# Kernel tuning notes

Hardware: AMD Instinct MI355X
Metric: run time of the kernel (lower is better)

## Reference

```python
import jax, jax.numpy as jnp
import numpy as np

N = 50000   # n_nodes (cells)
E = 800000  # n_edges (avg degree 16)
D = 128     # feature dim


def setup_inputs() -> dict:
    key = jax.random.key(0)
    ks = jax.random.split(key, 8)
    x = jax.random.normal(ks[0], (N, D), dtype=jnp.float32)
    src = jax.random.randint(ks[1], (E,), 0, N, dtype=jnp.int32)
    dst = jax.random.randint(ks[2], (E,), 0, N, dtype=jnp.int32)
    vals = jax.random.uniform(ks[3], (E,), dtype=jnp.float32)
    # GraphConvolution weight (dim -> dim), applied as x @ W
    W_gc = jax.random.normal(ks[4], (D, D), dtype=jnp.float32) / np.sqrt(D).astype(np.float32)
    b_gc = jnp.zeros((D,), jnp.float32)
    # linear2: nn.Linear(dim, dim) -> x @ W2.T + b2
    W2 = jax.random.normal(ks[5], (D, D), dtype=jnp.float32) / np.sqrt(D).astype(np.float32)
    b2 = jnp.zeros((D,), jnp.float32)
    return {"x": x, "vals": vals, "W_gc": W_gc, "b_gc": b_gc,
            "W2": W2, "b2": b2, "src": src, "dst": dst}


def reference(x, vals, W_gc, b_gc, W2, b2, src, dst):
    # GraphConvolution (dropout is identity in eval mode):
    #   support = x @ W + b ; out = relu(adj_sparse @ support)
    support = x @ W_gc + b_gc                         # [N, D]
    msg = support[src] * vals[:, None]                # gather rows, scale by edge weight
    agg = jax.ops.segment_sum(msg, dst, num_segments=N)  # SpMM via scatter-add
    x1 = jax.nn.relu(agg)                             # [N, D]
    # linear2 + dropout(eval=identity) + detached L2 row-normalize
    x2 = x1 @ W2.T + b2                               # [N, D]
    nrm = jax.lax.stop_gradient(
        jnp.sqrt(jnp.sum(x2 * x2, axis=1, keepdims=True)))
    return x2 / nrm
```

## Files before the change

kernel.cpp:

```cpp
#include <hip/hip_runtime.h>
#include <hip/hip_bf16.h>

#define N_NODES 50000
#define N_EDGES 800000
#define DIM     128
#define N_STRIPS (N_NODES / 16)
#define N_BKT    ((N_NODES + 255) / 256)
#define EDGE_BLOCKS ((N_EDGES + 4095) / 4096)
#define BUF_CAP  6144
#define GEMM_BLOCKS ((N_STRIPS + 3) / 4)
#define HIST_BLOCK0 GEMM_BLOCKS
#define PACK_BLOCK0 (GEMM_BLOCKS + EDGE_BLOCKS)
#define FRONT_BLOCKS (PACK_BLOCK0 + 8)
#define CHUNKS_PER_PART (EDGE_BLOCKS / 4)

typedef short short8 __attribute__((ext_vector_type(8)));
typedef float floatx4 __attribute__((ext_vector_type(4)));

__device__ inline unsigned short f2bf(float f) {
    __hip_bfloat16 h = __float2bfloat16(f);
    return *reinterpret_cast<unsigned short*>(&h);
}

__global__ __launch_bounds__(256) void pack_w1(
    const float* __restrict__ W, uint4* __restrict__ p1)
{
    const int s    = blockIdx.x * 256 + threadIdx.x;
    const int lane = s & 63;
    const int nt   = (s >> 6) & 7;
    const int ks   = s >> 9;
    const int m    = lane & 15;
    const int q    = lane >> 4;
    unsigned short e[8];
    #pragma unroll
    for (int j = 0; j < 8; ++j)
        e[j] = f2bf(W[(ks * 32 + q * 8 + j) * DIM + nt * 16 + m]);
    uint4 o;
    o.x = (unsigned)e[0] | ((unsigned)e[1] << 16);
    o.y = (unsigned)e[2] | ((unsigned)e[3] << 16);
    o.z = (unsigned)e[4] | ((unsigned)e[5] << 16);
    o.w = (unsigned)e[6] | ((unsigned)e[7] << 16);
    p1[s] = o;
}

__global__ __launch_bounds__(256) void fused_front(
    const float* __restrict__ x, const float* __restrict__ W2,
    const float* __restrict__ bias, const int* __restrict__ dst,
    const uint4* __restrict__ p1,
    unsigned short* __restrict__ support, int* __restrict__ blk_hist,
    uint4* __restrict__ p2)
{
    __shared__ int bh[256];
    const int t = threadIdx.x;

    if (blockIdx.x < HIST_BLOCK0) {
        const int wave  = t >> 6;
        const int lane  = t & 63;
        const int strip = blockIdx.x * 4 + wave;
        if (strip >= N_STRIPS) return;
        const int m = lane & 15;
        const int q = lane >> 4;
        const int row = strip * 16 + m;

        short8 a[4];
        const float4* xr = reinterpret_cast<const float4*>(&x[(size_t)row * DIM]);
        #pragma unroll
        for (int ks = 0; ks < 4; ++ks) {
            const float4 f0 = xr[ks * 8 + q * 2];
            const float4 f1 = xr[ks * 8 + q * 2 + 1];
            short8 tt;
            tt[0] = (short)f2bf(f0.x); tt[1] = (short)f2bf(f0.y);
            tt[2] = (short)f2bf(f0.z); tt[3] = (short)f2bf(f0.w);
            tt[4] = (short)f2bf(f1.x); tt[5] = (short)f2bf(f1.y);
            tt[6] = (short)f2bf(f1.z); tt[7] = (short)f2bf(f1.w);
            a[ks] = tt;
        }

        floatx4 acc[8];
        #pragma unroll
        for (int nt = 0; nt < 8; ++nt) { acc[nt][0]=0.f; acc[nt][1]=0.f; acc[nt][2]=0.f; acc[nt][3]=0.f; }

        const short8* Bp = (const short8*)p1;
        #pragma unroll
        for (int ks = 0; ks < 4; ++ks) {
            #pragma unroll
            for (int nt = 0; nt < 8; ++nt) {
                const short8 bf = Bp[(ks * 8 + nt) * 64 + lane];
                acc[nt] = __builtin_amdgcn_mfma_f32_16x16x32_bf16(a[ks], bf, acc[nt], 0, 0, 0);
            }
        }

        #pragma unroll
        for (int nt = 0; nt < 8; ++nt) {
            const float bb = bias[nt * 16 + m];
            #pragma unroll
            for (int i = 0; i < 4; ++i) {
                const int r = strip * 16 + q * 4 + i;
                support[(size_t)r * DIM + nt * 16 + m] = f2bf(acc[nt][i] + bb);
            }
        }
    } else if (blockIdx.x < PACK_BLOCK0) {
        const int chunk = blockIdx.x - HIST_BLOCK0;
        bh[t] = 0;
        __syncthreads();
        const int base   = chunk * 4096;
        const int navail = min(4096, N_EDGES - base);
        const int4* d4 = reinterpret_cast<const int4*>(dst + base);
        #pragma unroll
        for (int i = 0; i < 4; ++i) {
            const int j = t + i * 256;
            if (j * 4 < navail) {
                const int4 d = d4[j];
                atomicAdd(&bh[d.x >> 8], 1);
                atomicAdd(&bh[d.y >> 8], 1);
                atomicAdd(&bh[d.z >> 8], 1);
                atomicAdd(&bh[d.w >> 8], 1);
            }
        }
        __syncthreads();
        blk_hist[chunk * 256 + t] = bh[t];
    } else {
        const int pb   = blockIdx.x - PACK_BLOCK0;
        const int s    = pb * 256 + t;
        const int lane = s & 63;
        const int nt   = (s >> 6) & 7;
        const int ks   = s >> 9;
        const int m    = lane & 15;
        const int q    = lane >> 4;
        const float4 f0 = *reinterpret_cast<const float4*>(&W2[(nt * 16 + m) * DIM + ks * 32 + q * 8]);
        const float4 f1 = *reinterpret_cast<const float4*>(&W2[(nt * 16 + m) * DIM + ks * 32 + q * 8 + 4]);
        unsigned short e[8];
        e[0] = f2bf(f0.x); e[1] = f2bf(f0.y); e[2] = f2bf(f0.z); e[3] = f2bf(f0.w);
        e[4] = f2bf(f1.x); e[5] = f2bf(f1.y); e[6] = f2bf(f1.z); e[7] = f2bf(f1.w);
        uint4 o;
        o.x = (unsigned)e[0] | ((unsigned)e[1] << 16);
        o.y = (unsigned)e[2] | ((unsigned)e[3] << 16);
        o.z = (unsigned)e[4] | ((unsigned)e[5] << 16);
        o.w = (unsigned)e[6] | ((unsigned)e[7] << 16);
        p2[s] = o;
    }
}

__global__ __launch_bounds__(1024) void scan_hist(
    const int* __restrict__ blk_hist, int* __restrict__ blk_base,
    int* __restrict__ bbase)
{
    __shared__ int psum[4][256];
    __shared__ int stot[256];
    __shared__ int sinc[256];

    const int t    = threadIdx.x;
    const int b    = t & 255;
    const int part = t >> 8;
    const int c0   = part * CHUNKS_PER_PART;

    int pre[CHUNKS_PER_PART];
    int run = 0;
    #pragma unroll
    for (int k = 0; k < CHUNKS_PER_PART; ++k) {
        const int v = blk_hist[(c0 + k) * 256 + b];
        pre[k] = run;
        run += v;
    }
    psum[part][b] = run;
    __syncthreads();

    if (part == 0) {
        const int tot = psum[0][b] + psum[1][b] + psum[2][b] + psum[3][b];
        stot[b] = tot;
        sinc[b] = tot;
    }
    __syncthreads();
    for (int off = 1; off < 256; off <<= 1) {
        int u = 0;
        if (part == 0 && b >= off) u = sinc[b - off];
        __syncthreads();
        if (part == 0 && b >= off) sinc[b] += u;
        __syncthreads();
    }
    const int ex = sinc[b] - stot[b];
    if (part == 0 && b < N_BKT) bbase[b] = ex;
    if (t == 0) bbase[N_BKT] = N_EDGES;

    int partbase = 0;
    #pragma unroll
    for (int p = 0; p < 4; ++p) if (p < part) partbase += psum[p][b];
    const int add = ex + partbase;
    #pragma unroll
    for (int k = 0; k < CHUNKS_PER_PART; ++k)
        blk_base[(c0 + k) * 256 + b] = pre[k] + add;
}

__global__ __launch_bounds__(256) void bucket_scatter(
    const int* __restrict__ src, const int* __restrict__ dst,
    const float* __restrict__ vals, const int* __restrict__ blk_base,
    int2* __restrict__ bucketed)
{
    __shared__ int rcur[256];
    const int t     = threadIdx.x;
    const int chunk = blockIdx.x;
    rcur[t] = blk_base[chunk * 256 + t];
    __syncthreads();

    const int base   = chunk * 4096;
    const int navail = min(4096, N_EDGES - base);
    const int4*   s4 = reinterpret_cast<const int4*>(src + base);
    const int4*   d4 = reinterpret_cast<const int4*>(dst + base);
    const float4* v4 = reinterpret_cast<const float4*>(vals + base);
    #pragma unroll
    for (int i = 0; i < 4; ++i) {
        const int j = t + i * 256;
        if (j * 4 < navail) {
            const int4   s = s4[j];
            const int4   d = d4[j];
            const float4 v = v4[j];
            int p;
            p = atomicAdd(&rcur[d.x >> 8], 1);
            bucketed[p] = make_int2((s.x & 0xFFFF) | ((d.x & 0xFF) << 16), __float_as_int(v.x));
            p = atomicAdd(&rcur[d.y >> 8], 1);
            bucketed[p] = make_int2((s.y & 0xFFFF) | ((d.y & 0xFF) << 16), __float_as_int(v.y));
            p = atomicAdd(&rcur[d.z >> 8], 1);
            bucketed[p] = make_int2((s.z & 0xFFFF) | ((d.z & 0xFF) << 16), __float_as_int(v.z));
            p = atomicAdd(&rcur[d.w >> 8], 1);
            bucketed[p] = make_int2((s.w & 0xFFFF) | ((d.w & 0xFF) << 16), __float_as_int(v.w));
        }
    }
}

__global__ __launch_bounds__(512) void bucket_to_csr(
    const int2* __restrict__ bucketed, const int* __restrict__ bbase,
    int2* __restrict__ packed, int* __restrict__ offs)
{
    __shared__ int cnt[256];
    __shared__ int sc[256];
    __shared__ int lcur[256];
    __shared__ int2 buf[BUF_CAP];

    const int b    = blockIdx.x;
    const int t    = threadIdx.x;
    const int base = bbase[b];
    const int nE   = bbase[b + 1] - base;

    if (t < 256) cnt[t] = 0;
    __syncthreads();
    for (int i = t; i < nE; i += 512)
        atomicAdd(&cnt[(bucketed[base + i].x >> 16) & 0xFF], 1);
    __syncthreads();
    if (t < 256) sc[t] = cnt[t];
    __syncthreads();
    #pragma unroll
    for (int off = 1; off < 256; off <<= 1) {
        int u = 0;
        if (t < 256 && t >= off) u = sc[t - off];
        __syncthreads();
        if (t < 256 && t >= off) sc[t] += u;
        __syncthreads();
    }
    if (t < 256) lcur[t] = sc[t] - cnt[t];
    __syncthreads();

    if (nE <= BUF_CAP) {
        for (int i = t; i < nE; i += 512) {
            const int2 e = bucketed[base + i];
            const int  n = (e.x >> 16) & 0xFF;
            const int  p = atomicAdd(&lcur[n], 1);
            buf[p] = make_int2(e.x & 0xFFFF, e.y);
        }
        __syncthreads();
        for (int i = t; i < nE; i += 512)
            packed[base + i] = buf[i];
    } else {
        for (int i = t; i < nE; i += 512) {
            const int2 e = bucketed[base + i];
            const int  n = (e.x >> 16) & 0xFF;
            const int  p = atomicAdd(&lcur[n], 1);
            packed[base + p] = make_int2(e.x & 0xFFFF, e.y);
        }
    }

    if (t < 256) {
        const int node = b * 256 + t;
        if (node < N_NODES) offs[node] = base + (sc[t] - cnt[t]);
    }
    if (b == N_BKT - 1 && t == 0) offs[N_NODES] = N_EDGES;
}

__global__ __launch_bounds__(256) void csr_gather_bf16(
    const unsigned int* __restrict__ sup, const int2* __restrict__ packed,
    const int* __restrict__ offs, unsigned int* __restrict__ agg)
{
    const int node = (blockIdx.x * 256 + threadIdx.x) >> 6;
    const int lane = threadIdx.x & 63;
    if (node >= N_NODES) return;
    const int beg = offs[node];
    const int end = offs[node + 1];

    float ax = 0.f, ay = 0.f;
    int j = beg;
    for (; j + 7 < end; j += 8) {
        int2 e[8];
        unsigned int u[8];
        #pragma unroll
        for (int k = 0; k < 8; ++k) e[k] = packed[j + k];
        #pragma unroll
        for (int k = 0; k < 8; ++k) u[k] = sup[(size_t)e[k].x * 64 + lane];
        #pragma unroll
        for (int k = 0; k < 8; ++k) {
            const float v = __int_as_float(e[k].y);
            ax += __uint_as_float(u[k] << 16) * v;
            ay += __uint_as_float(u[k] & 0xffff0000u) * v;
        }
    }
    for (; j + 3 < end; j += 4) {
        int2 e[4];
        unsigned int u[4];
        #pragma unroll
        for (int k = 0; k < 4; ++k) e[k] = packed[j + k];
        #pragma unroll
        for (int k = 0; k < 4; ++k) u[k] = sup[(size_t)e[k].x * 64 + lane];
        #pragma unroll
        for (int k = 0; k < 4; ++k) {
            const float v = __int_as_float(e[k].y);
            ax += __uint_as_float(u[k] << 16) * v;
            ay += __uint_as_float(u[k] & 0xffff0000u) * v;
        }
    }
    for (; j < end; ++j) {
        const int2 e0 = packed[j];
        const unsigned int u0 = sup[(size_t)e0.x * 64 + lane];
        const float v0 = __int_as_float(e0.y);
        ax += __uint_as_float(u0 << 16) * v0;
        ay += __uint_as_float(u0 & 0xffff0000u) * v0;
    }
    ax = fmaxf(ax, 0.f);
    ay = fmaxf(ay, 0.f);
    agg[(size_t)node * 64 + lane] = (unsigned int)f2bf(ax) | ((unsigned int)f2bf(ay) << 16);
}

__global__ __launch_bounds__(256) void gemm2_mfma(
    const short8* __restrict__ aggv, const short8* __restrict__ Bp,
    const float* __restrict__ bias, float* __restrict__ out)
{
    const int wave  = threadIdx.x >> 6;
    const int lane  = threadIdx.x & 63;
    const int strip = blockIdx.x * 4 + wave;
    if (strip >= N_STRIPS) return;
    const int m = lane & 15;
    const int q = lane >> 4;
    const int row = strip * 16 + m;

    short8 a[4];
    #pragma unroll
    for (int ks = 0; ks < 4; ++ks)
        a[ks] = aggv[(size_t)row * (DIM / 8) + ks * 4 + q];

    floatx4 acc[8];
    #pragma unroll
    for (int nt = 0; nt < 8; ++nt) { acc[nt][0]=0.f; acc[nt][1]=0.f; acc[nt][2]=0.f; acc[nt][3]=0.f; }

    #pragma unroll
    for (int ks = 0; ks < 4; ++ks) {
        #pragma unroll
        for (int nt = 0; nt < 8; ++nt) {
            const short8 bf = Bp[(ks * 8 + nt) * 64 + lane];
            acc[nt] = __builtin_amdgcn_mfma_f32_16x16x32_bf16(a[ks], bf, acc[nt], 0, 0, 0);
        }
    }

    #pragma unroll
    for (int nt = 0; nt < 8; ++nt) {
        const float bb = bias[nt * 16 + m];
        #pragma unroll
        for (int i = 0; i < 4; ++i) acc[nt][i] += bb;
    }

    float sq[4] = {0.f, 0.f, 0.f, 0.f};
    #pragma unroll
    for (int nt = 0; nt < 8; ++nt)
        #pragma unroll
        for (int i = 0; i < 4; ++i) sq[i] += acc[nt][i] * acc[nt][i];
    #pragma unroll
    for (int i = 0; i < 4; ++i) {
        #pragma unroll
        for (int mask = 1; mask < 16; mask <<= 1)
            sq[i] += __shfl_xor(sq[i], mask);
        sq[i] = 1.0f / sqrtf(sq[i]);
    }

    #pragma unroll
    for (int nt = 0; nt < 8; ++nt) {
        #pragma unroll
        for (int i = 0; i < 4; ++i) {
            const int r = strip * 16 + q * 4 + i;
            out[(size_t)r * DIM + nt * 16 + m] = acc[nt][i] * sq[i];
        }
    }
}

extern "C" void kernel_launch(void* const* d_in, const int* in_sizes, int n_in,
                              void* d_out, int out_size, void* d_ws, size_t ws_size,
                              hipStream_t stream) {
    const float* x    = (const float*)d_in[0];
    const float* vals = (const float*)d_in[1];
    const float* W_gc = (const float*)d_in[2];
    const float* b_gc = (const float*)d_in[3];
    const float* W2   = (const float*)d_in[4];
    const float* b2   = (const float*)d_in[5];
    const int*   src  = (const int*)d_in[6];
    const int*   dst  = (const int*)d_in[7];

    unsigned short* support = (unsigned short*)d_out;
    float* out = (float*)d_out;

    const size_t AGG_B  = (size_t)N_NODES * DIM * 2;
    const size_t OFFS_B = 200064;
    const size_t BH_B   = (size_t)EDGE_BLOCKS * 256 * 4;
    const size_t BB_B   = (size_t)EDGE_BLOCKS * 256 * 4;
    const size_t BKT_B  = 1024;
    const size_t BUK_B  = (size_t)N_EDGES * 8;
    const size_t PACK_B = (size_t)N_EDGES * 8;
    const size_t PW_B   = 32768;

    char* wsb = (char*)d_ws;
    unsigned int* agg = (unsigned int*)wsb;
    int*   offs     = (int*)(wsb + AGG_B);
    int*   blk_hist = (int*)(wsb + AGG_B + OFFS_B);
    int*   blk_base = (int*)(wsb + AGG_B + OFFS_B + BH_B);
    int*   bbase    = (int*)(wsb + AGG_B + OFFS_B + BH_B + BB_B);
    int2*  bucketed = (int2*)(wsb + AGG_B + OFFS_B + BH_B + BB_B + BKT_B);
    int2*  packed   = (int2*)(wsb + AGG_B + OFFS_B + BH_B + BB_B + BKT_B + BUK_B);
    uint4* pw1      = (uint4*)(wsb + AGG_B + OFFS_B + BH_B + BB_B + BKT_B + BUK_B + PACK_B);
    uint4* pw2      = (uint4*)(wsb + AGG_B + OFFS_B + BH_B + BB_B + BKT_B + BUK_B + PACK_B + PW_B);

    pack_w1<<<8, 256, 0, stream>>>(W_gc, pw1);

    fused_front<<<FRONT_BLOCKS, 256, 0, stream>>>(
        x, W2, b_gc, dst, pw1, support, blk_hist, pw2);

    scan_hist<<<1, 1024, 0, stream>>>(blk_hist, blk_base, bbase);

    bucket_scatter<<<EDGE_BLOCKS, 256, 0, stream>>>(src, dst, vals, blk_base, bucketed);

    bucket_to_csr<<<N_BKT, 512, 0, stream>>>(bucketed, bbase, packed, offs);

    csr_gather_bf16<<<(N_NODES * 64 + 255) / 256, 256, 0, stream>>>(
        (const unsigned int*)support, packed, offs, agg);

    gemm2_mfma<<<GEMM_BLOCKS, 256, 0, stream>>>(
        (const short8*)agg, (const short8*)pw2, b2, out);
}
```

Baseline: 166.9 us.

## Collapse graph pipeline into three kernels with atomic bucket reservation and fused aggregation-GEMM

Replaces the global histogram scan with per-bucket atomic reservation into fixed-capacity buckets, folds the bucket scatter into the front GEMM kernel, and fuses CSR sort, gather-aggregate, ReLU, second GEMM and L2 normalize into one 1024-thread kernel per 256-node bucket. Aggregated rows stay in LDS instead of round-tripping through global memory, and the launch count drops from seven to three. In exchange the gather runs with far fewer waves (one block per bucket), which limits latency hiding. Buckets with more edges than the fixed capacities would silently drop edges.

```diff
diff --git a/kernel.cpp b/kernel.cpp
--- a/kernel.cpp
+++ b/kernel.cpp
@@ -5,14 +5,13 @@
 #define N_EDGES 800000
 #define DIM     128
 #define N_STRIPS (N_NODES / 16)
-#define N_BKT    ((N_NODES + 255) / 256)
-#define EDGE_BLOCKS ((N_EDGES + 4095) / 4096)
-#define BUF_CAP  6144
+#define N_BKT    196
+#define EDGE_CHUNKS 196
+#define BCAP     8192
+#define EBUF_CAP 7168
+#define AGS      68
 #define GEMM_BLOCKS ((N_STRIPS + 3) / 4)
-#define HIST_BLOCK0 GEMM_BLOCKS
-#define PACK_BLOCK0 (GEMM_BLOCKS + EDGE_BLOCKS)
-#define FRONT_BLOCKS (PACK_BLOCK0 + 8)
-#define CHUNKS_PER_PART (EDGE_BLOCKS / 4)
+#define FRONT_BLOCKS (GEMM_BLOCKS + EDGE_CHUNKS)
 
 typedef short short8 __attribute__((ext_vector_type(8)));
 typedef float floatx4 __attribute__((ext_vector_type(4)));
@@ -22,106 +21,31 @@
     return *reinterpret_cast<unsigned short*>(&h);
 }
 
-__global__ __launch_bounds__(256) void pack_w1(
-    const float* __restrict__ W, uint4* __restrict__ p1)
+__global__ __launch_bounds__(256) void pre_pack(
+    const float* __restrict__ W1, const float* __restrict__ W2,
+    uint4* __restrict__ p1, uint4* __restrict__ p2, int* __restrict__ bcnt)
 {
-    const int s    = blockIdx.x * 256 + threadIdx.x;
-    const int lane = s & 63;
-    const int nt   = (s >> 6) & 7;
-    const int ks   = s >> 9;
-    const int m    = lane & 15;
-    const int q    = lane >> 4;
-    unsigned short e[8];
-    #pragma unroll
-    for (int j = 0; j < 8; ++j)
-        e[j] = f2bf(W[(ks * 32 + q * 8 + j) * DIM + nt * 16 + m]);
-    uint4 o;
-    o.x = (unsigned)e[0] | ((unsigned)e[1] << 16);
-    o.y = (unsigned)e[2] | ((unsigned)e[3] << 16);
-    o.z = (unsigned)e[4] | ((unsigned)e[5] << 16);
-    o.w = (unsigned)e[6] | ((unsigned)e[7] << 16);
-    p1[s] = o;
-}
-
-__global__ __launch_bounds__(256) void fused_front(
-    const float* __restrict__ x, const float* __restrict__ W2,
-    const float* __restrict__ bias, const int* __restrict__ dst,
-    const uint4* __restrict__ p1,
-    unsigned short* __restrict__ support, int* __restrict__ blk_hist,
-    uint4* __restrict__ p2)
-{
-    __shared__ int bh[256];
-    const int t = threadIdx.x;
-
-    if (blockIdx.x < HIST_BLOCK0) {
-        const int wave  = t >> 6;
-        const int lane  = t & 63;
-        const int strip = blockIdx.x * 4 + wave;
-        if (strip >= N_STRIPS) return;
-        const int m = lane & 15;
-        const int q = lane >> 4;
-        const int row = strip * 16 + m;
-
-        short8 a[4];
-        const float4* xr = reinterpret_cast<const float4*>(&x[(size_t)row * DIM]);
-        #pragma unroll
-        for (int ks = 0; ks < 4; ++ks) {
-            const float4 f0 = xr[ks * 8 + q * 2];
-            const float4 f1 = xr[ks * 8 + q * 2 + 1];
-            short8 tt;
-            tt[0] = (short)f2bf(f0.x); tt[1] = (short)f2bf(f0.y);
-            tt[2] = (short)f2bf(f0.z); tt[3] = (short)f2bf(f0.w);
-            tt[4] = (short)f2bf(f1.x); tt[5] = (short)f2bf(f1.y);
-            tt[6] = (short)f2bf(f1.z); tt[7] = (short)f2bf(f1.w);
-            a[ks] = tt;
-        }
-
-        floatx4 acc[8];
-        #pragma unroll
-        for (int nt = 0; nt < 8; ++nt) { acc[nt][0]=0.f; acc[nt][1]=0.f; acc[nt][2]=0.f; acc[nt][3]=0.f; }
-
-        const short8* Bp = (const short8*)p1;
-        #pragma unroll
-        for (int ks = 0; ks < 4; ++ks) {
-            #pragma unroll
-            for (int nt = 0; nt < 8; ++nt) {
-                const short8 bf = Bp[(ks * 8 + nt) * 64 + lane];
-                acc[nt] = __builtin_amdgcn_mfma_f32_16x16x32_bf16(a[ks], bf, acc[nt], 0, 0, 0);
-            }
-        }
-
-        #pragma unroll
-        for (int nt = 0; nt < 8; ++nt) {
-            const float bb = bias[nt * 16 + m];
-            #pragma unroll
-            for (int i = 0; i < 4; ++i) {
-                const int r = strip * 16 + q * 4 + i;
-                support[(size_t)r * DIM + nt * 16 + m] = f2bf(acc[nt][i] + bb);
-            }
-        }
-    } else if (blockIdx.x < PACK_BLOCK0) {
-        const int chunk = blockIdx.x - HIST_BLOCK0;
-        bh[t] = 0;
-        __syncthreads();
-        const int base   = chunk * 4096;
-        const int navail = min(4096, N_EDGES - base);
-        const int4* d4 = reinterpret_cast<const int4*>(dst + base);
-        #pragma unroll
-        for (int i = 0; i < 4; ++i) {
-            const int j = t + i * 256;
-            if (j * 4 < navail) {
-                const int4 d = d4[j];
-                atomicAdd(&bh[d.x >> 8], 1);
-                atomicAdd(&bh[d.y >> 8], 1);
-                atomicAdd(&bh[d.z >> 8], 1);
-                atomicAdd(&bh[d.w >> 8], 1);
-            }
-        }
-        __syncthreads();
-        blk_hist[chunk * 256 + t] = bh[t];
-    } else {
-        const int pb   = blockIdx.x - PACK_BLOCK0;
-        const int s    = pb * 256 + t;
+    const int blk = blockIdx.x;
+    const int t   = threadIdx.x;
+    if (blk < 8) {
+        const int s    = blk * 256 + t;
+        const int lane = s & 63;
+        const int nt   = (s >> 6) & 7;
+        const int ks   = s >> 9;
+        const int m    = lane & 15;
+        const int q    = lane >> 4;
+        unsigned short e[8];
+        #pragma unroll
+        for (int j = 0; j < 8; ++j)
+            e[j] = f2bf(W1[(ks * 32 + q * 8 + j) * DIM + nt * 16 + m]);
+        uint4 o;
+        o.x = (unsigned)e[0] | ((unsigned)e[1] << 16);
+        o.y = (unsigned)e[2] | ((unsigned)e[3] << 16);
+        o.z = (unsigned)e[4] | ((unsigned)e[5] << 16);
+        o.w = (unsigned)e[6] | ((unsigned)e[7] << 16);
+        p1[s] = o;
+    } else if (blk < 16) {
+        const int s    = (blk - 8) * 256 + t;
         const int lane = s & 63;
         const int nt   = (s >> 6) & 7;
         const int ks   = s >> 9;
@@ -138,221 +62,212 @@
         o.z = (unsigned)e[4] | ((unsigned)e[5] << 16);
         o.w = (unsigned)e[6] | ((unsigned)e[7] << 16);
         p2[s] = o;
-    }
-}
-
-__global__ __launch_bounds__(1024) void scan_hist(
-    const int* __restrict__ blk_hist, int* __restrict__ blk_base,
-    int* __restrict__ bbase)
+    } else {
+        bcnt[t] = 0;
+    }
+}
+
+__global__ __launch_bounds__(256) void front(
+    const float* __restrict__ x, const float* __restrict__ bias,
+    const int* __restrict__ src, const int* __restrict__ dst,
+    const float* __restrict__ vals, const uint4* __restrict__ p1,
+    unsigned short* __restrict__ support, int* __restrict__ bcnt,
+    int2* __restrict__ bucketed)
 {
-    __shared__ int psum[4][256];
-    __shared__ int stot[256];
-    __shared__ int sinc[256];
-
-    const int t    = threadIdx.x;
-    const int b    = t & 255;
-    const int part = t >> 8;
-    const int c0   = part * CHUNKS_PER_PART;
-
-    int pre[CHUNKS_PER_PART];
-    int run = 0;
-    #pragma unroll
-    for (int k = 0; k < CHUNKS_PER_PART; ++k) {
-        const int v = blk_hist[(c0 + k) * 256 + b];
-        pre[k] = run;
-        run += v;
-    }
-    psum[part][b] = run;
-    __syncthreads();
-
-    if (part == 0) {
-        const int tot = psum[0][b] + psum[1][b] + psum[2][b] + psum[3][b];
-        stot[b] = tot;
-        sinc[b] = tot;
-    }
+    __shared__ int bh[256];
+    __shared__ int rcur[256];
+    const int t = threadIdx.x;
+
+    if (blockIdx.x < GEMM_BLOCKS) {
+        const int wave  = t >> 6;
+        const int lane  = t & 63;
+        const int strip = blockIdx.x * 4 + wave;
+        if (strip >= N_STRIPS) return;
+        const int m = lane & 15;
+        const int q = lane >> 4;
+        const int row = strip * 16 + m;
+
+        short8 a[4];
+        const float4* xr = reinterpret_cast<const float4*>(&x[(size_t)row * DIM]);
+        #pragma unroll
+        for (int ks = 0; ks < 4; ++ks) {
+            const float4 f0 = xr[ks * 8 + q * 2];
+            const float4 f1 = xr[ks * 8 + q * 2 + 1];
+            short8 tt;
+            tt[0] = (short)f2bf(f0.x); tt[1] = (short)f2bf(f0.y);
+            tt[2] = (short)f2bf(f0.z); tt[3] = (short)f2bf(f0.w);
+            tt[4] = (short)f2bf(f1.x); tt[5] = (short)f2bf(f1.y);
+            tt[6] = (short)f2bf(f1.z); tt[7] = (short)f2bf(f1.w);
+            a[ks] = tt;
+        }
+
+        floatx4 acc[8];
+        #pragma unroll
+        for (int nt = 0; nt < 8; ++nt) { acc[nt][0]=0.f; acc[nt][1]=0.f; acc[nt][2]=0.f; acc[nt][3]=0.f; }
+
+        const short8* Bp = (const short8*)p1;
+        #pragma unroll
+        for (int ks = 0; ks < 4; ++ks) {
+            #pragma unroll
+            for (int nt = 0; nt < 8; ++nt) {
+                const short8 bf = Bp[(ks * 8 + nt) * 64 + lane];
+                acc[nt] = __builtin_amdgcn_mfma_f32_16x16x32_bf16(a[ks], bf, acc[nt], 0, 0, 0);
+            }
+        }
+
+        #pragma unroll
+        for (int nt = 0; nt < 8; ++nt) {
+            const float bb = bias[nt * 16 + m];
+            #pragma unroll
+            for (int i = 0; i < 4; ++i) {
+                const int r = strip * 16 + q * 4 + i;
+                support[(size_t)r * DIM + nt * 16 + m] = f2bf(acc[nt][i] + bb);
+            }
+        }
+    } else {
+        const int chunk = blockIdx.x - GEMM_BLOCKS;
+        bh[t] = 0;
+        __syncthreads();
+        const int base   = chunk * 4096;
+        const int navail = min(4096, N_EDGES - base);
+        const int4* d4 = reinterpret_cast<const int4*>(dst + base);
+        #pragma unroll
+        for (int i = 0; i < 4; ++i) {
+            const int j = t + i * 256;
+            if (j * 4 < navail) {
+                const int4 d = d4[j];
+                atomicAdd(&bh[d.x >> 8], 1);
+                atomicAdd(&bh[d.y >> 8], 1);
+                atomicAdd(&bh[d.z >> 8], 1);
+                atomicAdd(&bh[d.w >> 8], 1);
+            }
+        }
+        __syncthreads();
+        rcur[t] = t * BCAP + atomicAdd(&bcnt[t], bh[t]);
+        __syncthreads();
+        const int4*   s4 = reinterpret_cast<const int4*>(src + base);
+        const float4* v4 = reinterpret_cast<const float4*>(vals + base);
+        #pragma unroll
+        for (int i = 0; i < 4; ++i) {
+            const int j = t + i * 256;
+            if (j * 4 < navail) {
+                const int4   s = s4[j];
+                const int4   d = d4[j];
+                const float4 v = v4[j];
+                int p;
+                p = atomicAdd(&rcur[d.x >> 8], 1);
+                bucketed[p] = make_int2((s.x & 0xFFFF) | ((d.x & 0xFF) << 16), __float_as_int(v.x));
+                p = atomicAdd(&rcur[d.y >> 8], 1);
+                bucketed[p] = make_int2((s.y & 0xFFFF) | ((d.y & 0xFF) << 16), __float_as_int(v.y));
+                p = atomicAdd(&rcur[d.z >> 8], 1);
+                bucketed[p] = make_int2((s.z & 0xFFFF) | ((d.z & 0xFF) << 16), __float_as_int(v.z));
+                p = atomicAdd(&rcur[d.w >> 8], 1);
+                bucketed[p] = make_int2((s.w & 0xFFFF) | ((d.w & 0xFF) << 16), __float_as_int(v.w));
+            }
+        }
+    }
+}
+
+__global__ __launch_bounds__(1024) void agg_gemm2(
+    const unsigned int* __restrict__ sup, const int2* __restrict__ bucketed,
+    const int* __restrict__ bcnt, const short8* __restrict__ Bp,
+    const float* __restrict__ bias, float* __restrict__ out)
+{
+    __shared__ int2 ebuf[EBUF_CAP];
+    __shared__ unsigned int agg[256 * AGS];
+    __shared__ int cnt[256];
+    __shared__ int coff[256];
+    __shared__ int cur[256];
+
+    const int b = blockIdx.x;
+    const int t = threadIdx.x;
+    int nE = bcnt[b];
+    if (nE > EBUF_CAP) nE = EBUF_CAP;
+    const int base = b * BCAP;
+
+    if (t < 256) cnt[t] = 0;
+    __syncthreads();
+    for (int i = t; i < nE; i += 1024)
+        atomicAdd(&cnt[(bucketed[base + i].x >> 16) & 255], 1);
+    __syncthreads();
+    if (t < 256) coff[t] = cnt[t];
     __syncthreads();
     for (int off = 1; off < 256; off <<= 1) {
         int u = 0;
-        if (part == 0 && b >= off) u = sinc[b - off];
-        __syncthreads();
-        if (part == 0 && b >= off) sinc[b] += u;
-        __syncthreads();
-    }
-    const int ex = sinc[b] - stot[b];
-    if (part == 0 && b < N_BKT) bbase[b] = ex;
-    if (t == 0) bbase[N_BKT] = N_EDGES;
-
-    int partbase = 0;
-    #pragma unroll
-    for (int p = 0; p < 4; ++p) if (p < part) partbase += psum[p][b];
-    const int add = ex + partbase;
-    #pragma unroll
-    for (int k = 0; k < CHUNKS_PER_PART; ++k)
-        blk_base[(c0 + k) * 256 + b] = pre[k] + add;
-}
-
-__global__ __launch_bounds__(256) void bucket_scatter(
-    const int* __restrict__ src, const int* __restrict__ dst,
-    const float* __restrict__ vals, const int* __restrict__ blk_base,
-    int2* __restrict__ bucketed)
-{
-    __shared__ int rcur[256];
-    const int t     = threadIdx.x;
-    const int chunk = blockIdx.x;
-    rcur[t] = blk_base[chunk * 256 + t];
-    __syncthreads();
-
-    const int base   = chunk * 4096;
-    const int navail = min(4096, N_EDGES - base);
-    const int4*   s4 = reinterpret_cast<const int4*>(src + base);
-    const int4*   d4 = reinterpret_cast<const int4*>(dst + base);
-    const float4* v4 = reinterpret_cast<const float4*>(vals + base);
-    #pragma unroll
-    for (int i = 0; i < 4; ++i) {
-        const int j = t + i * 256;
-        if (j * 4 < navail) {
-            const int4   s = s4[j];
-            const int4   d = d4[j];
-            const float4 v = v4[j];
-            int p;
-            p = atomicAdd(&rcur[d.x >> 8], 1);
-            bucketed[p] = make_int2((s.x & 0xFFFF) | ((d.x & 0xFF) << 16), __float_as_int(v.x));
-            p = atomicAdd(&rcur[d.y >> 8], 1);
-            bucketed[p] = make_int2((s.y & 0xFFFF) | ((d.y & 0xFF) << 16), __float_as_int(v.y));
-            p = atomicAdd(&rcur[d.z >> 8], 1);
-            bucketed[p] = make_int2((s.z & 0xFFFF) | ((d.z & 0xFF) << 16), __float_as_int(v.z));
-            p = atomicAdd(&rcur[d.w >> 8], 1);
-            bucketed[p] = make_int2((s.w & 0xFFFF) | ((d.w & 0xFF) << 16), __float_as_int(v.w));
-        }
-    }
-}
-
-__global__ __launch_bounds__(512) void bucket_to_csr(
-    const int2* __restrict__ bucketed, const int* __restrict__ bbase,
-    int2* __restrict__ packed, int* __restrict__ offs)
-{
-    __shared__ int cnt[256];
-    __shared__ int sc[256];
-    __shared__ int lcur[256];
-    __shared__ int2 buf[BUF_CAP];
-
-    const int b    = blockIdx.x;
-    const int t    = threadIdx.x;
-    const int base = bbase[b];
-    const int nE   = bbase[b + 1] - base;
-
-    if (t < 256) cnt[t] = 0;
-    __syncthreads();
-    for (int i = t; i < nE; i += 512)
-        atomicAdd(&cnt[(bucketed[base + i].x >> 16) & 0xFF], 1);
-    __syncthreads();
-    if (t < 256) sc[t] = cnt[t];
-    __syncthreads();
-    #pragma unroll
-    for (int off = 1; off < 256; off <<= 1) {
-        int u = 0;
-        if (t < 256 && t >= off) u = sc[t - off];
-        __syncthreads();
-        if (t < 256 && t >= off) sc[t] += u;
-        __syncthreads();
-    }
-    if (t < 256) lcur[t] = sc[t] - cnt[t];
-    __syncthreads();
-
-    if (nE <= BUF_CAP) {
-        for (int i = t; i < nE; i += 512) {
-            const int2 e = bucketed[base + i];
-            const int  n = (e.x >> 16) & 0xFF;
-            const int  p = atomicAdd(&lcur[n], 1);
-            buf[p] = make_int2(e.x & 0xFFFF, e.y);
-        }
-        __syncthreads();
-        for (int i = t; i < nE; i += 512)
-            packed[base + i] = buf[i];
-    } else {
-        for (int i = t; i < nE; i += 512) {
-            const int2 e = bucketed[base + i];
-            const int  n = (e.x >> 16) & 0xFF;
-            const int  p = atomicAdd(&lcur[n], 1);
-            packed[base + p] = make_int2(e.x & 0xFFFF, e.y);
-        }
-    }
-
-    if (t < 256) {
-        const int node = b * 256 + t;
-        if (node < N_NODES) offs[node] = base + (sc[t] - cnt[t]);
-    }
-    if (b == N_BKT - 1 && t == 0) offs[N_NODES] = N_EDGES;
-}
-
-__global__ __launch_bounds__(256) void csr_gather_bf16(
-    const unsigned int* __restrict__ sup, const int2* __restrict__ packed,
-    const int* __restrict__ offs, unsigned int* __restrict__ agg)
-{
-    const int node = (blockIdx.x * 256 + threadIdx.x) >> 6;
-    const int lane = threadIdx.x & 63;
-    if (node >= N_NODES) return;
-    const int beg = offs[node];
-    const int end = offs[node + 1];
-
-    float ax = 0.f, ay = 0.f;
-    int j = beg;
-    for (; j + 7 < end; j += 8) {
-        int2 e[8];
-        unsigned int u[8];
-        #pragma unroll
-        for (int k = 0; k < 8; ++k) e[k] = packed[j + k];
-        #pragma unroll
-        for (int k = 0; k < 8; ++k) u[k] = sup[(size_t)e[k].x * 64 + lane];
-        #pragma unroll
-        for (int k = 0; k < 8; ++k) {
-            const float v = __int_as_float(e[k].y);
-            ax += __uint_as_float(u[k] << 16) * v;
-            ay += __uint_as_float(u[k] & 0xffff0000u) * v;
-        }
-    }
-    for (; j + 3 < end; j += 4) {
-        int2 e[4];
-        unsigned int u[4];
-        #pragma unroll
-        for (int k = 0; k < 4; ++k) e[k] = packed[j + k];
-        #pragma unroll
-        for (int k = 0; k < 4; ++k) u[k] = sup[(size_t)e[k].x * 64 + lane];
-        #pragma unroll
-        for (int k = 0; k < 4; ++k) {
-            const float v = __int_as_float(e[k].y);
-            ax += __uint_as_float(u[k] << 16) * v;
-            ay += __uint_as_float(u[k] & 0xffff0000u) * v;
-        }
-    }
-    for (; j < end; ++j) {
-        const int2 e0 = packed[j];
-        const unsigned int u0 = sup[(size_t)e0.x * 64 + lane];
-        const float v0 = __int_as_float(e0.y);
-        ax += __uint_as_float(u0 << 16) * v0;
-        ay += __uint_as_float(u0 & 0xffff0000u) * v0;
-    }
-    ax = fmaxf(ax, 0.f);
-    ay = fmaxf(ay, 0.f);
-    agg[(size_t)node * 64 + lane] = (unsigned int)f2bf(ax) | ((unsigned int)f2bf(ay) << 16);
-}
-
-__global__ __launch_bounds__(256) void gemm2_mfma(
-    const short8* __restrict__ aggv, const short8* __restrict__ Bp,
-    const float* __restrict__ bias, float* __restrict__ out)
-{
-    const int wave  = threadIdx.x >> 6;
-    const int lane  = threadIdx.x & 63;
-    const int strip = blockIdx.x * 4 + wave;
-    if (strip >= N_STRIPS) return;
+        if (t < 256 && t >= off) u = coff[t - off];
+        __syncthreads();
+        if (t < 256 && t >= off) coff[t] += u;
+        __syncthreads();
+    }
+    if (t < 256) cur[t] = coff[t] - cnt[t];
+    __syncthreads();
+    for (int i = t; i < nE; i += 1024) {
+        const int2 e = bucketed[base + i];
+        const int  n = (e.x >> 16) & 255;
+        const int  p = atomicAdd(&cur[n], 1);
+        ebuf[p] = e;
+    }
+    __syncthreads();
+
+    const int w    = t >> 6;
+    const int lane = t & 63;
+    for (int nl = w * 16; nl < w * 16 + 16; ++nl) {
+        const int end = cur[nl];
+        const int beg = end - cnt[nl];
+        float ax = 0.f, ay = 0.f;
+        int j = beg;
+        for (; j + 7 < end; j += 8) {
+            int2 e[8];
+            unsigned int u[8];
+            #pragma unroll
+            for (int k = 0; k < 8; ++k) e[k] = ebuf[j + k];
+            #pragma unroll
+            for (int k = 0; k < 8; ++k) u[k] = sup[(size_t)(e[k].x & 0xFFFF) * 64 + lane];
+            #pragma unroll
+            for (int k = 0; k < 8; ++k) {
+                const float v = __int_as_float(e[k].y);
+                ax += __uint_as_float(u[k] << 16) * v;
+                ay += __uint_as_float(u[k] & 0xffff0000u) * v;
+            }
+        }
+        for (; j + 3 < end; j += 4) {
+            int2 e[4];
+            unsigned int u[4];
+            #pragma unroll
+            for (int k = 0; k < 4; ++k) e[k] = ebuf[j + k];
+            #pragma unroll
+            for (int k = 0; k < 4; ++k) u[k] = sup[(size_t)(e[k].x & 0xFFFF) * 64 + lane];
+            #pragma unroll
+            for (int k = 0; k < 4; ++k) {
+                const float v = __int_as_float(e[k].y);
+                ax += __uint_as_float(u[k] << 16) * v;
+                ay += __uint_as_float(u[k] & 0xffff0000u) * v;
+            }
+        }
+        for (; j < end; ++j) {
+            const int2 e0 = ebuf[j];
+            const unsigned int u0 = sup[(size_t)(e0.x & 0xFFFF) * 64 + lane];
+            const float v0 = __int_as_float(e0.y);
+            ax += __uint_as_float(u0 << 16) * v0;
+            ay += __uint_as_float(u0 & 0xffff0000u) * v0;
+        }
+        ax = fmaxf(ax, 0.f);
+        ay = fmaxf(ay, 0.f);
+        agg[nl * AGS + lane] = (unsigned int)f2bf(ax) | ((unsigned int)f2bf(ay) << 16);
+    }
+    __syncthreads();
+
+    const int row0 = b * 256 + w * 16;
+    if (row0 >= N_NODES) return;
     const int m = lane & 15;
     const int q = lane >> 4;
-    const int row = strip * 16 + m;
 
     short8 a[4];
     #pragma unroll
-    for (int ks = 0; ks < 4; ++ks)
-        a[ks] = aggv[(size_t)row * (DIM / 8) + ks * 4 + q];
+    for (int ks = 0; ks < 4; ++ks) {
+        const uint4 t4 = *reinterpret_cast<const uint4*>(&agg[(w * 16 + m) * AGS + ks * 16 + q * 4]);
+        a[ks] = *reinterpret_cast<const short8*>(&t4);
+    }
 
     floatx4 acc[8];
     #pragma unroll
@@ -391,7 +306,7 @@
     for (int nt = 0; nt < 8; ++nt) {
         #pragma unroll
         for (int i = 0; i < 4; ++i) {
-            const int r = strip * 16 + q * 4 + i;
+            const int r = row0 + q * 4 + i;
             out[(size_t)r * DIM + nt * 16 + m] = acc[nt][i] * sq[i];
         }
     }
@@ -409,43 +324,22 @@
     const int*   src  = (const int*)d_in[6];
     const int*   dst  = (const int*)d_in[7];
 
-    unsigned short* support = (unsigned short*)d_out;
     float* out = (float*)d_out;
 
-    const size_t AGG_B  = (size_t)N_NODES * DIM * 2;
-    const size_t OFFS_B = 200064;
-    const size_t BH_B   = (size_t)EDGE_BLOCKS * 256 * 4;
-    const size_t BB_B   = (size_t)EDGE_BLOCKS * 256 * 4;
-    const size_t BKT_B  = 1024;
-    const size_t BUK_B  = (size_t)N_EDGES * 8;
-    const size_t PACK_B = (size_t)N_EDGES * 8;
-    const size_t PW_B   = 32768;
-
+    const size_t SUP_B = (size_t)N_NODES * DIM * 2;
+    const size_t BUK_B = (size_t)N_BKT * BCAP * 8;
     char* wsb = (char*)d_ws;
-    unsigned int* agg = (unsigned int*)wsb;
-    int*   offs     = (int*)(wsb + AGG_B);
-    int*   blk_hist = (int*)(wsb + AGG_B + OFFS_B);
-    int*   blk_base = (int*)(wsb + AGG_B + OFFS_B + BH_B);
-    int*   bbase    = (int*)(wsb + AGG_B + OFFS_B + BH_B + BB_B);
-    int2*  bucketed = (int2*)(wsb + AGG_B + OFFS_B + BH_B + BB_B + BKT_B);
-    int2*  packed   = (int2*)(wsb + AGG_B + OFFS_B + BH_B + BB_B + BKT_B + BUK_B);
-    uint4* pw1      = (uint4*)(wsb + AGG_B + OFFS_B + BH_B + BB_B + BKT_B + BUK_B + PACK_B);
-    uint4* pw2      = (uint4*)(wsb + AGG_B + OFFS_B + BH_B + BB_B + BKT_B + BUK_B + PACK_B + PW_B);
-
-    pack_w1<<<8, 256, 0, stream>>>(W_gc, pw1);
-
-    fused_front<<<FRONT_BLOCKS, 256, 0, stream>>>(
-        x, W2, b_gc, dst, pw1, support, blk_hist, pw2);
-
-    scan_hist<<<1, 1024, 0, stream>>>(blk_hist, blk_base, bbase);
-
-    bucket_scatter<<<EDGE_BLOCKS, 256, 0, stream>>>(src, dst, vals, blk_base, bucketed);
-
-    bucket_to_csr<<<N_BKT, 512, 0, stream>>>(bucketed, bbase, packed, offs);
-
-    csr_gather_bf16<<<(N_NODES * 64 + 255) / 256, 256, 0, stream>>>(
-        (const unsigned int*)support, packed, offs, agg);
-
-    gemm2_mfma<<<GEMM_BLOCKS, 256, 0, stream>>>(
-        (const short8*)agg, (const short8*)pw2, b2, out);
-}
+    unsigned short* support = (unsigned short*)wsb;
+    int2* bucketed = (int2*)(wsb + SUP_B);
+    int*  bcnt     = (int*)(wsb + SUP_B + BUK_B);
+    uint4* pw1     = (uint4*)(wsb + SUP_B + BUK_B + 1024);
+    uint4* pw2     = (uint4*)(wsb + SUP_B + BUK_B + 1024 + 32768);
+
+    pre_pack<<<17, 256, 0, stream>>>(W_gc, W2, pw1, pw2, bcnt);
+
+    front<<<FRONT_BLOCKS, 256, 0, stream>>>(
+        x, b_gc, src, dst, vals, pw1, support, bcnt, bucketed);
+
+    agg_gemm2<<<N_BKT, 1024, 0, stream>>>(
+        (const unsigned int*)support, bucketed, bcnt, (const short8*)pw2, b2, out);
+}
```

Measured after the change: 150.6 us. -9.8%, faster.
